# Optimization experiments

Hardware: AMD Instinct MI355X
Metric: run time of the kernel (lower is better)

## Reference

```python
import jax, jax.numpy as jnp
import numpy as np

IN_C = 256
OUT_C = 256
K_NUM = 6
EDGE_TYPE = 3


def setup_inputs() -> dict:
    key = jax.random.key(0)
    k1, k2, k3, k4, k5 = jax.random.split(key, 5)
    N, T, V = 32, 64, 25
    x = jax.random.normal(k1, (N, IN_C, T, V), dtype=jnp.float32)
    A = jax.random.uniform(k2, (K_NUM - EDGE_TYPE, V, V), dtype=jnp.float32)
    B = jax.random.uniform(k3, (N, EDGE_TYPE, V, V), dtype=jnp.float32)
    lamda_act = jnp.float32(0.5)
    # ConvTranspose2d with kernel (1,1), stride 1, no padding == pointwise matmul.
    # torch weight shape (in, out, 1, 1) -> store squeezed (in, out).
    W = jax.random.normal(k4, (IN_C, OUT_C * K_NUM), dtype=jnp.float32) * (1.0 / np.sqrt(IN_C))
    b = jax.random.normal(k5, (OUT_C * K_NUM,), dtype=jnp.float32) * 0.01
    return {"x": x, "A": A, "B": B, "lamda_act": lamda_act, "W": W, "b": b}


def reference(x, A, B, lamda_act, W, b):
    # pointwise transposed conv (1x1 kernel) -> channel matmul
    y = jnp.einsum('nctv,co->notv', x, W) + b[None, :, None, None]  # [N, K*C_out, T, V]
    n, kc, t, v = y.shape
    y = y.reshape(n, K_NUM, kc // K_NUM, t, v)
    x1 = jnp.einsum('nkctv,kvw->nctw', y[:, :K_NUM - EDGE_TYPE], A)
    x2 = jnp.einsum('nkctv,nkvw->nctw', y[:, K_NUM - EDGE_TYPE:], B)
    x_sum = x1 + x2 * lamda_act
    return (x_sum, A)
```

## Files before the change

### kernel.cpp

```cpp
#include <hip/hip_runtime.h>
#include <hip/hip_bf16.h>
#include <stdint.h>

typedef __bf16 bf16_t;
typedef bf16_t bf16x8 __attribute__((ext_vector_type(8)));
typedef float f32x4 __attribute__((ext_vector_type(4)));

#define DEVI static __device__ __forceinline__

constexpr int NB = 32, CIN = 256, COUT = 256, KNUM = 6, ET = 3, TDIM = 64, VV = 25;
constexpr int KD   = KNUM * CIN;
constexpr long OUT0 = (long)NB * COUT * TDIM * VV;
constexpr int ACNT = ET * VV * VV;

constexpr int NSTEP = 24;
constexpr int WP3_CHUNKS = NSTEP * 2048;
constexpr size_t WP3_BYTES  = (size_t)WP3_CHUNKS * 16;
constexpr size_t BIAS_OFF   = WP3_BYTES;
constexpr size_t BIAS_BYTES = (size_t)NB * VV * COUT * 4;
constexpr size_t WS_NEED    = BIAS_OFF + BIAS_BYTES;

DEVI unsigned packbf(float lo, float hi) {
  unsigned short a = __builtin_bit_cast(unsigned short, (bf16_t)lo);
  unsigned short b = __builtin_bit_cast(unsigned short, (bf16_t)hi);
  return ((unsigned)b << 16) | (unsigned)a;
}

__global__ __launch_bounds__(256) void prep_kernel(
    const float* __restrict__ A, const float* __restrict__ Bm,
    const float* __restrict__ lam_p, const float* __restrict__ W,
    const float* __restrict__ bvec, bf16_t* __restrict__ wp3,
    float* __restrict__ biasmat, float* __restrict__ outA)
{
  int idx = blockIdx.x * 256 + threadIdx.x;
  constexpr int S1 = WP3_CHUNKS;
  constexpr int S2 = S1 + NB * VV * COUT;
  constexpr int S3 = S2 + ACNT;
  if (idx < S1) {
    int s  = idx >> 11;
    int r  = idx & 2047;
    int mi = r >> 7;
    int kk = (r >> 6) & 1;
    int ln = r & 63;
    int lg = ln >> 4, lw = ln & 15;
    int cb = s / 6, k = s - cb * 6;
    int cibase = cb * 64 + (lg + 4 * kk) * 8;
    int col = (k << 8) + mi * 16 + lw;
    bf16_t* dst = wp3 + ((long)idx << 3);
    #pragma unroll
    for (int e = 0; e < 8; ++e)
      dst[e] = (bf16_t)W[(cibase + e) * KD + col];
  } else if (idx < S2) {
    int j = idx - S1;
    int c = j & 255;
    int nw = j >> 8;
    int w = nw % VV;
    int n = nw / VV;
    float lam = lam_p[0];
    float s = 0.f;
    for (int k = 0; k < KNUM; ++k) {
      float sk = 0.f;
      if (k < ET) {
        for (int v = 0; v < VV; ++v) sk += A[(k * VV + v) * VV + w];
      } else {
        for (int v = 0; v < VV; ++v) sk += Bm[(((n * ET) + (k - ET)) * VV + v) * VV + w];
        sk *= lam;
      }
      s += bvec[(k << 8) + c] * sk;
    }
    biasmat[j] = s;
  } else if (idx < S3) {
    int j = idx - S2;
    outA[j] = A[j];
  }
}

__global__ __launch_bounds__(512, 2) void fused_kernel(
    const float* __restrict__ x, const float* __restrict__ A,
    const float* __restrict__ Bm, const float* __restrict__ lam_p,
    const bf16_t* __restrict__ wp3, const float* __restrict__ biasmat,
    float* __restrict__ out)
{
  __shared__ bf16_t Bs[2 * 128 * 64];
  __shared__ bf16_t Xs[256 * 32];
  __shared__ bf16_t Ms[KNUM * 32 * 32];

  const int b = blockIdx.x;
  const int n = b >> 4;
  const int t0 = (b & 15) << 2;
  const int tid = threadIdx.x;
  const int wv = tid >> 6, ln = tid & 63;
  const int lw = ln & 15, lg = ln >> 4;
  const float lam = lam_p[0];

  for (int i = tid; i < KNUM * 32 * 32; i += 512) {
    int R = i >> 5, v = i & 31;
    int k = i >> 10, w = (i >> 5) & 31;
    float val = 0.f;
    if (w < VV && v < VV)
      val = (k < ET) ? A[(k * VV + v) * VV + w]
                     : lam * Bm[(((n * ET) + (k - ET)) * VV + v) * VV + w];
    int sw2 = (w & 3) ^ ((w >> 2) & 3);
    int byteoff = R * 64 + ((((v >> 3) ^ sw2) & 3) << 4) + ((v & 7) << 1);
    *(bf16_t*)((char*)Ms + byteoff) = (bf16_t)val;
  }

  f32x4 acc[4][4] = {};
  const int m_base = (wv >> 1) * 64;
  const int mb4 = (wv >> 1) * 4;
  const int n_base = (wv & 1) * 64;
  const f32x4 z4 = {0.f, 0.f, 0.f, 0.f};
  const int msw2 = (lw & 3) ^ ((lw >> 2) & 3);

  for (int cb = 0; cb < 4; ++cb) {
    if (tid < 256) {
      int ci = tid >> 2, dt = tid & 3;
      const float* xp = x + ((long)(n * CIN + cb * 64 + ci) * TDIM + t0 + dt) * VV;
      float xv[25];
      #pragma unroll
      for (int v = 0; v < VV; ++v) xv[v] = xp[v];
      int row = dt * 64 + ci;
      int sw = (row & 3) ^ ((row >> 2) & 3);
      #pragma unroll
      for (int g = 0; g < 4; ++g) {
        char* base = (char*)Xs + row * 64 + ((g ^ sw) & 3) * 16;
        #pragma unroll
        for (int p = 0; p < 4; ++p) {
          int v0 = g * 8 + p * 2;
          float lo = (v0     < VV) ? xv[v0 < VV ? v0 : 0]     : 0.f;
          float hi = (v0 + 1 < VV) ? xv[v0 + 1 < VV ? v0 + 1 : 0] : 0.f;
          *(unsigned*)(base + p * 4) = packbf(lo, hi);
        }
      }
    }
    __syncthreads();

    for (int k = 0; k < KNUM; ++k) {
      const int s = cb * 6 + k;
      const int buf = (s & 1) * (128 * 64);
      bf16x8 af2[2][4];
      const bf16_t* wpS = wp3 + (((long)s * 2048 + (long)mb4 * 128 + ln) << 3);
      #pragma unroll
      for (int kk = 0; kk < 2; ++kk)
        #pragma unroll
        for (int i = 0; i < 4; ++i)
          af2[kk][i] = *(const bf16x8*)(wpS + ((i * 128 + kk * 64) << 3));

      bf16x8 mb0 = *(const bf16x8*)((const char*)Ms + (k * 32 + lw) * 64 + (((lg ^ msw2) & 3) << 4));
      bf16x8 mb1 = *(const bf16x8*)((const char*)Ms + (k * 32 + 16 + lw) * 64 + (((lg ^ msw2) & 3) << 4));
      #pragma unroll
      for (int rt = 0; rt < 2; ++rt) {
        int arow = wv * 32 + rt * 16 + lw;
        int sw = (arow & 3) ^ ((arow >> 2) & 3);
        bf16x8 af = *(const bf16x8*)((const char*)Xs + arow * 64 + ((lg ^ sw) & 3) * 16);
        f32x4 d0 = __builtin_amdgcn_mfma_f32_16x16x32_bf16(af, mb0, z4, 0, 0, 0);
        f32x4 d1 = __builtin_amdgcn_mfma_f32_16x16x32_bf16(af, mb1, z4, 0, 0, 0);
        int rbase = wv * 32 + rt * 16 + (lg << 2);
        int dt = rbase >> 6, ci0 = rbase & 63;
        int r0 = dt * 32 + lw;
        int g0 = ((ci0 >> 3) ^ (r0 & 7)) & 7;
        char* c0 = (char*)(Bs + buf) + r0 * 128 + (g0 << 4) + ((ci0 << 1) & 15);
        *(unsigned*)(c0)     = packbf(d0[0], d0[1]);
        *(unsigned*)(c0 + 4) = packbf(d0[2], d0[3]);
        int r1 = r0 + 16;
        char* c1 = (char*)(Bs + buf) + r1 * 128 + (g0 << 4) + ((ci0 << 1) & 15);
        *(unsigned*)(c1)     = packbf(d1[0], d1[1]);
        *(unsigned*)(c1 + 4) = packbf(d1[2], d1[3]);
      }
      __syncthreads();

      __builtin_amdgcn_s_setprio(1);
      #pragma unroll
      for (int kk = 0; kk < 2; ++kk) {
        bf16x8 bf2[4];
        #pragma unroll
        for (int j = 0; j < 4; ++j) {
          int rr = n_base + j * 16 + lw;
          int gg = ((kk * 4 + lg) ^ (rr & 7)) & 7;
          bf2[j] = *(const bf16x8*)((const char*)(Bs + buf) + rr * 128 + (gg << 4));
        }
        #pragma unroll
        for (int i = 0; i < 4; ++i)
          #pragma unroll
          for (int j = 0; j < 4; ++j)
            acc[i][j] = __builtin_amdgcn_mfma_f32_16x16x32_bf16(af2[kk][i], bf2[j], acc[i][j], 0, 0, 0);
      }
      __builtin_amdgcn_s_setprio(0);
    }
  }

  #pragma unroll
  for (int j = 0; j < 4; ++j) {
    int colb = n_base + j * 16 + lw;
    int dt = colb >> 5, w = colb & 31;
    if (w < VV) {
      float* ob = out + (long)n * 409600 + (t0 + dt) * 25 + w;
      const float* brow = biasmat + (n * 25 + w) * 256;
      #pragma unroll
      for (int i = 0; i < 4; ++i) {
        int mb = m_base + i * 16 + (lg << 2);
        #pragma unroll
        for (int r = 0; r < 4; ++r) {
          int m = mb + r;
          ob[(long)m * 1600] = acc[i][j][r] + brow[m];
        }
      }
    }
  }
}

__global__ __launch_bounds__(256) void fallback_kernel(
    const float* __restrict__ x, const float* __restrict__ A,
    const float* __restrict__ Bm, const float* __restrict__ lam_p,
    const float* __restrict__ W, const float* __restrict__ bvec,
    float* __restrict__ out)
{
  __shared__ __align__(16) float xs[CIN][28];
  __shared__ __align__(16) float Ms[KNUM][VV][28];
  const int nt = blockIdx.x;
  const int n = nt >> 6, t = nt & 63;
  const int tid = threadIdx.x;
  const float lam = lam_p[0];

  const float* xp = x + (((long)(n * CIN + tid) * TDIM + t) * VV);
  #pragma unroll
  for (int v = 0; v < VV; ++v) xs[tid][v] = xp[v];
  xs[tid][25] = xs[tid][26] = xs[tid][27] = 0.f;
  for (int i = tid; i < KNUM * VV * VV; i += 256) {
    int k = i / (VV * VV);
    int r = i - k * VV * VV;
    int v = r / VV;
    int w = r - v * VV;
    Ms[k][v][w] = (k < ET) ? A[(k * VV + v) * VV + w]
                           : lam * Bm[(((n * ET) + (k - ET)) * VV + v) * VV + w];
    if (w == 24) { Ms[k][v][25] = Ms[k][v][26] = Ms[k][v][27] = 0.f; }
  }
  __syncthreads();

  float oacc[28] = {};
  for (int k = 0; k < KNUM; ++k) {
    float yv[28];
    float bv = bvec[(k << 8) + tid];
    #pragma unroll
    for (int v = 0; v < 28; ++v) yv[v] = 0.f;
    for (int ci = 0; ci < CIN; ++ci) {
      float wl = W[ci * KD + (k << 8) + tid];
      const f32x4* x4 = (const f32x4*)&xs[ci][0];
      #pragma unroll
      for (int q = 0; q < 7; ++q) {
        f32x4 xv = x4[q];
        yv[q*4+0] += wl*xv[0]; yv[q*4+1] += wl*xv[1];
        yv[q*4+2] += wl*xv[2]; yv[q*4+3] += wl*xv[3];
      }
    }
    #pragma unroll
    for (int v = 0; v < VV; ++v) {
      float yvv = yv[v] + bv;
      const f32x4* m4 = (const f32x4*)&Ms[k][v][0];
      #pragma unroll
      for (int q = 0; q < 7; ++q) {
        f32x4 mv = m4[q];
        oacc[q*4+0] += yvv*mv[0]; oacc[q*4+1] += yvv*mv[1];
        oacc[q*4+2] += yvv*mv[2]; oacc[q*4+3] += yvv*mv[3];
      }
    }
  }
  float* op = out + (((long)(n * COUT + tid) * TDIM + t) * VV);
  #pragma unroll
  for (int w = 0; w < VV; ++w) op[w] = oacc[w];
}

__global__ void copyA_kernel(const float* __restrict__ A, float* __restrict__ outA) {
  int i = blockIdx.x * 256 + threadIdx.x;
  if (i < ACNT) outA[i] = A[i];
}

extern "C" void kernel_launch(void* const* d_in, const int* in_sizes, int n_in,
                              void* d_out, int out_size, void* d_ws, size_t ws_size,
                              hipStream_t stream) {
  const float* x   = (const float*)d_in[0];
  const float* A   = (const float*)d_in[1];
  const float* Bm  = (const float*)d_in[2];
  const float* lam = (const float*)d_in[3];
  const float* W   = (const float*)d_in[4];
  const float* bv  = (const float*)d_in[5];
  float* out = (float*)d_out;

  if (d_ws != nullptr && ws_size >= WS_NEED) {
    bf16_t* wp3     = (bf16_t*)d_ws;
    float*  biasmat = (float*)((char*)d_ws + BIAS_OFF);
    constexpr int PREP_ITEMS = WP3_CHUNKS + NB * VV * COUT + ACNT;
    prep_kernel<<<(PREP_ITEMS + 255) / 256, 256, 0, stream>>>(A, Bm, lam, W, bv, wp3, biasmat, out + OUT0);
    fused_kernel<<<NB * 16, 512, 0, stream>>>(x, A, Bm, lam, wp3, biasmat, out);
  } else {
    fallback_kernel<<<NB * TDIM, 256, 0, stream>>>(x, A, Bm, lam, W, bv, out);
    copyA_kernel<<<(ACNT + 255) / 256, 256, 0, stream>>>(A, out + OUT0);
  }
}
```

Measured before the change: 84.55 us.

## Feed first-stage MFMA outputs directly as B-fragments, removing Bs LDS round trip

Each wave now recomputes the graph-mixing MFMA (X times adjacency) for exactly the columns it needs and repacks the fp32 results into bf16 B-operand fragments in registers. This drops the Bs shared-memory staging buffer and the per-step __syncthreads, and Xs rows are permuted so the accumulator layout lines up with the operand layout. The cost is redundant first-stage MFMAs: both waves sharing an n-range recompute the same tile, roughly doubling that small stage. Weight fragments are now loaded per kk, and the k loop is kept rolled.

```diff
diff --git a/kernel.cpp b/kernel.cpp
--- a/kernel.cpp
+++ b/kernel.cpp
@@ -24,6 +24,13 @@
   unsigned short a = __builtin_bit_cast(unsigned short, (bf16_t)lo);
   unsigned short b = __builtin_bit_cast(unsigned short, (bf16_t)hi);
   return ((unsigned)b << 16) | (unsigned)a;
+}
+
+DEVI bf16x8 pack8(f32x4 a, f32x4 b) {
+  union { unsigned u[4]; bf16x8 v; } u;
+  u.u[0] = packbf(a[0], a[1]); u.u[1] = packbf(a[2], a[3]);
+  u.u[2] = packbf(b[0], b[1]); u.u[3] = packbf(b[2], b[3]);
+  return u.v;
 }
 
 __global__ __launch_bounds__(256) void prep_kernel(
@@ -81,7 +88,6 @@
     const bf16_t* __restrict__ wp3, const float* __restrict__ biasmat,
     float* __restrict__ out)
 {
-  __shared__ bf16_t Bs[2 * 128 * 64];
   __shared__ bf16_t Xs[256 * 32];
   __shared__ bf16_t Ms[KNUM * 32 * 32];
 
@@ -109,17 +115,20 @@
   const int m_base = (wv >> 1) * 64;
   const int mb4 = (wv >> 1) * 4;
   const int n_base = (wv & 1) * 64;
+  const int dtb = (wv & 1) * 2;
   const f32x4 z4 = {0.f, 0.f, 0.f, 0.f};
   const int msw2 = (lw & 3) ^ ((lw >> 2) & 3);
 
   for (int cb = 0; cb < 4; ++cb) {
+    __syncthreads();
     if (tid < 256) {
       int ci = tid >> 2, dt = tid & 3;
       const float* xp = x + ((long)(n * CIN + cb * 64 + ci) * TDIM + t0 + dt) * VV;
       float xv[25];
       #pragma unroll
       for (int v = 0; v < VV; ++v) xv[v] = xp[v];
-      int row = dt * 64 + ci;
+      int kk = ci >> 5, rem = ci & 31, q = rem >> 3, r = rem & 7;
+      int row = dt * 64 + kk * 32 + (r >> 2) * 16 + q * 4 + (r & 3);
       int sw = (row & 3) ^ ((row >> 2) & 3);
       #pragma unroll
       for (int g = 0; g < 4; ++g) {
@@ -135,57 +144,44 @@
     }
     __syncthreads();
 
+    #pragma unroll 1
     for (int k = 0; k < KNUM; ++k) {
       const int s = cb * 6 + k;
-      const int buf = (s & 1) * (128 * 64);
-      bf16x8 af2[2][4];
-      const bf16_t* wpS = wp3 + (((long)s * 2048 + (long)mb4 * 128 + ln) << 3);
-      #pragma unroll
-      for (int kk = 0; kk < 2; ++kk)
-        #pragma unroll
-        for (int i = 0; i < 4; ++i)
-          af2[kk][i] = *(const bf16x8*)(wpS + ((i * 128 + kk * 64) << 3));
-
       bf16x8 mb0 = *(const bf16x8*)((const char*)Ms + (k * 32 + lw) * 64 + (((lg ^ msw2) & 3) << 4));
       bf16x8 mb1 = *(const bf16x8*)((const char*)Ms + (k * 32 + 16 + lw) * 64 + (((lg ^ msw2) & 3) << 4));
-      #pragma unroll
-      for (int rt = 0; rt < 2; ++rt) {
-        int arow = wv * 32 + rt * 16 + lw;
-        int sw = (arow & 3) ^ ((arow >> 2) & 3);
-        bf16x8 af = *(const bf16x8*)((const char*)Xs + arow * 64 + ((lg ^ sw) & 3) * 16);
-        f32x4 d0 = __builtin_amdgcn_mfma_f32_16x16x32_bf16(af, mb0, z4, 0, 0, 0);
-        f32x4 d1 = __builtin_amdgcn_mfma_f32_16x16x32_bf16(af, mb1, z4, 0, 0, 0);
-        int rbase = wv * 32 + rt * 16 + (lg << 2);
-        int dt = rbase >> 6, ci0 = rbase & 63;
-        int r0 = dt * 32 + lw;
-        int g0 = ((ci0 >> 3) ^ (r0 & 7)) & 7;
-        char* c0 = (char*)(Bs + buf) + r0 * 128 + (g0 << 4) + ((ci0 << 1) & 15);
-        *(unsigned*)(c0)     = packbf(d0[0], d0[1]);
-        *(unsigned*)(c0 + 4) = packbf(d0[2], d0[3]);
-        int r1 = r0 + 16;
-        char* c1 = (char*)(Bs + buf) + r1 * 128 + (g0 << 4) + ((ci0 << 1) & 15);
-        *(unsigned*)(c1)     = packbf(d1[0], d1[1]);
-        *(unsigned*)(c1 + 4) = packbf(d1[2], d1[3]);
-      }
-      __syncthreads();
-
-      __builtin_amdgcn_s_setprio(1);
+      const bf16_t* wpS = wp3 + (((long)s * 2048 + (long)mb4 * 128 + ln) << 3);
+
       #pragma unroll
       for (int kk = 0; kk < 2; ++kk) {
-        bf16x8 bf2[4];
-        #pragma unroll
-        for (int j = 0; j < 4; ++j) {
-          int rr = n_base + j * 16 + lw;
-          int gg = ((kk * 4 + lg) ^ (rr & 7)) & 7;
-          bf2[j] = *(const bf16x8*)((const char*)(Bs + buf) + rr * 128 + (gg << 4));
+        bf16x8 af2[4];
+        #pragma unroll
+        for (int i = 0; i < 4; ++i)
+          af2[i] = *(const bf16x8*)(wpS + ((i * 128 + kk * 64) << 3));
+
+        bf16x8 bfrag[4];
+        #pragma unroll
+        for (int dtl = 0; dtl < 2; ++dtl) {
+          int ra = (dtb + dtl) * 64 + kk * 32 + lw;
+          int swa = (ra & 3) ^ ((ra >> 2) & 3);
+          int off = ((lg ^ swa) & 3) << 4;
+          bf16x8 afa = *(const bf16x8*)((const char*)Xs + ra * 64 + off);
+          bf16x8 afb = *(const bf16x8*)((const char*)Xs + (ra + 16) * 64 + off);
+          f32x4 da0 = __builtin_amdgcn_mfma_f32_16x16x32_bf16(afa, mb0, z4, 0, 0, 0);
+          f32x4 db0 = __builtin_amdgcn_mfma_f32_16x16x32_bf16(afb, mb0, z4, 0, 0, 0);
+          f32x4 da1 = __builtin_amdgcn_mfma_f32_16x16x32_bf16(afa, mb1, z4, 0, 0, 0);
+          f32x4 db1 = __builtin_amdgcn_mfma_f32_16x16x32_bf16(afb, mb1, z4, 0, 0, 0);
+          bfrag[dtl * 2 + 0] = pack8(da0, db0);
+          bfrag[dtl * 2 + 1] = pack8(da1, db1);
         }
+
+        __builtin_amdgcn_s_setprio(1);
         #pragma unroll
         for (int i = 0; i < 4; ++i)
           #pragma unroll
           for (int j = 0; j < 4; ++j)
-            acc[i][j] = __builtin_amdgcn_mfma_f32_16x16x32_bf16(af2[kk][i], bf2[j], acc[i][j], 0, 0, 0);
-      }
-      __builtin_amdgcn_s_setprio(0);
+            acc[i][j] = __builtin_amdgcn_mfma_f32_16x16x32_bf16(af2[i], bfrag[j], acc[i][j], 0, 0, 0);
+        __builtin_amdgcn_s_setprio(0);
+      }
     }
   }
 
```

New measurement: 94.75 us. 1.12x slower.

## Split output channels across two blocks and stage epilogue through LDS for coalesced stores

Applied to the files above, without the earlier changes.

Doubles the grid so each block computes half of the 256 output channels, halving accumulator registers and raising launch bounds to 4 waves-per-SIMD occupancy. The x tile load is spread across all 512 threads instead of 256. The epilogue now stages accumulators through shared memory and writes contiguous runs of the output, replacing strided per-element stores. In exchange, the first-stage x·M product and the x load are recomputed by both halves, so that work is duplicated.

```diff
diff --git a/kernel.cpp b/kernel.cpp
--- a/kernel.cpp
+++ b/kernel.cpp
@@ -75,19 +75,21 @@
   }
 }
 
-__global__ __launch_bounds__(512, 2) void fused_kernel(
+__global__ __launch_bounds__(512, 4) void fused_kernel(
     const float* __restrict__ x, const float* __restrict__ A,
     const float* __restrict__ Bm, const float* __restrict__ lam_p,
     const bf16_t* __restrict__ wp3, const float* __restrict__ biasmat,
     float* __restrict__ out)
 {
-  __shared__ bf16_t Bs[2 * 128 * 64];
-  __shared__ bf16_t Xs[256 * 32];
-  __shared__ bf16_t Ms[KNUM * 32 * 32];
+  __shared__ __align__(16) bf16_t Bs[2 * 128 * 64];
+  __shared__ __align__(16) bf16_t Xs[256 * 32];
+  __shared__ __align__(16) bf16_t Ms[KNUM * 32 * 32];
 
   const int b = blockIdx.x;
-  const int n = b >> 4;
-  const int t0 = (b & 15) << 2;
+  const int half = b >> 9;
+  const int rest = b & 511;
+  const int n = rest >> 4;
+  const int t0 = (rest & 15) << 2;
   const int tid = threadIdx.x;
   const int wv = tid >> 6, ln = tid & 63;
   const int lw = ln & 15, lg = ln >> 4;
@@ -105,45 +107,53 @@
     *(bf16_t*)((char*)Ms + byteoff) = (bf16_t)val;
   }
 
-  f32x4 acc[4][4] = {};
-  const int m_base = (wv >> 1) * 64;
-  const int mb4 = (wv >> 1) * 4;
+  f32x4 acc[2][4] = {};
+  const int miB = half * 8 + (wv >> 1) * 2;
   const int n_base = (wv & 1) * 64;
   const f32x4 z4 = {0.f, 0.f, 0.f, 0.f};
   const int msw2 = (lw & 3) ^ ((lw >> 2) & 3);
 
   for (int cb = 0; cb < 4; ++cb) {
-    if (tid < 256) {
-      int ci = tid >> 2, dt = tid & 3;
-      const float* xp = x + ((long)(n * CIN + cb * 64 + ci) * TDIM + t0 + dt) * VV;
-      float xv[25];
-      #pragma unroll
-      for (int v = 0; v < VV; ++v) xv[v] = xp[v];
+    __syncthreads();
+    {
+      int jj = tid & 255, gh = tid >> 8;
+      int ci = jj >> 2, dt = jj & 3;
+      const float* xp = x + ((long)(n * CIN + cb * 64 + ci) * TDIM + t0 + dt) * VV + gh * 16;
+      float xv[16];
+      #pragma unroll
+      for (int v = 0; v < 16; ++v) xv[v] = 0.f;
+      if (gh == 0) {
+        #pragma unroll
+        for (int v = 0; v < 16; ++v) xv[v] = xp[v];
+      } else {
+        #pragma unroll
+        for (int v = 0; v < 9; ++v) xv[v] = xp[v];
+      }
       int row = dt * 64 + ci;
       int sw = (row & 3) ^ ((row >> 2) & 3);
       #pragma unroll
-      for (int g = 0; g < 4; ++g) {
+      for (int g2 = 0; g2 < 2; ++g2) {
+        int g = gh * 2 + g2;
         char* base = (char*)Xs + row * 64 + ((g ^ sw) & 3) * 16;
         #pragma unroll
         for (int p = 0; p < 4; ++p) {
-          int v0 = g * 8 + p * 2;
-          float lo = (v0     < VV) ? xv[v0 < VV ? v0 : 0]     : 0.f;
-          float hi = (v0 + 1 < VV) ? xv[v0 + 1 < VV ? v0 + 1 : 0] : 0.f;
-          *(unsigned*)(base + p * 4) = packbf(lo, hi);
+          int vl = g2 * 8 + p * 2;
+          *(unsigned*)(base + p * 4) = packbf(xv[vl], xv[vl + 1]);
         }
       }
     }
     __syncthreads();
 
+    #pragma unroll 1
     for (int k = 0; k < KNUM; ++k) {
       const int s = cb * 6 + k;
       const int buf = (s & 1) * (128 * 64);
-      bf16x8 af2[2][4];
-      const bf16_t* wpS = wp3 + (((long)s * 2048 + (long)mb4 * 128 + ln) << 3);
+      bf16x8 af2[2][2];
+      const bf16_t* wpS = wp3 + (((long)s * 2048 + (long)miB * 128 + ln) << 3);
       #pragma unroll
       for (int kk = 0; kk < 2; ++kk)
         #pragma unroll
-        for (int i = 0; i < 4; ++i)
+        for (int i = 0; i < 2; ++i)
           af2[kk][i] = *(const bf16x8*)(wpS + ((i * 128 + kk * 64) << 3));
 
       bf16x8 mb0 = *(const bf16x8*)((const char*)Ms + (k * 32 + lw) * 64 + (((lg ^ msw2) & 3) << 4));
@@ -152,20 +162,18 @@
       for (int rt = 0; rt < 2; ++rt) {
         int arow = wv * 32 + rt * 16 + lw;
         int sw = (arow & 3) ^ ((arow >> 2) & 3);
-        bf16x8 af = *(const bf16x8*)((const char*)Xs + arow * 64 + ((lg ^ sw) & 3) * 16);
+        int off = ((lg ^ sw) & 3) << 4;
+        bf16x8 af = *(const bf16x8*)((const char*)Xs + arow * 64 + off);
         f32x4 d0 = __builtin_amdgcn_mfma_f32_16x16x32_bf16(af, mb0, z4, 0, 0, 0);
         f32x4 d1 = __builtin_amdgcn_mfma_f32_16x16x32_bf16(af, mb1, z4, 0, 0, 0);
         int rbase = wv * 32 + rt * 16 + (lg << 2);
         int dt = rbase >> 6, ci0 = rbase & 63;
         int r0 = dt * 32 + lw;
         int g0 = ((ci0 >> 3) ^ (r0 & 7)) & 7;
-        char* c0 = (char*)(Bs + buf) + r0 * 128 + (g0 << 4) + ((ci0 << 1) & 15);
-        *(unsigned*)(c0)     = packbf(d0[0], d0[1]);
-        *(unsigned*)(c0 + 4) = packbf(d0[2], d0[3]);
-        int r1 = r0 + 16;
-        char* c1 = (char*)(Bs + buf) + r1 * 128 + (g0 << 4) + ((ci0 << 1) & 15);
-        *(unsigned*)(c1)     = packbf(d1[0], d1[1]);
-        *(unsigned*)(c1 + 4) = packbf(d1[2], d1[3]);
+        uint2 p0; p0.x = packbf(d0[0], d0[1]); p0.y = packbf(d0[2], d0[3]);
+        *(uint2*)((char*)(Bs + buf) + r0 * 128 + (g0 << 4) + ((ci0 << 1) & 15)) = p0;
+        uint2 p1; p1.x = packbf(d1[0], d1[1]); p1.y = packbf(d1[2], d1[3]);
+        *(uint2*)((char*)(Bs + buf) + (r0 + 16) * 128 + (g0 << 4) + ((ci0 << 1) & 15)) = p1;
       }
       __syncthreads();
 
@@ -180,7 +188,7 @@
           bf2[j] = *(const bf16x8*)((const char*)(Bs + buf) + rr * 128 + (gg << 4));
         }
         #pragma unroll
-        for (int i = 0; i < 4; ++i)
+        for (int i = 0; i < 2; ++i)
           #pragma unroll
           for (int j = 0; j < 4; ++j)
             acc[i][j] = __builtin_amdgcn_mfma_f32_16x16x32_bf16(af2[kk][i], bf2[j], acc[i][j], 0, 0, 0);
@@ -189,23 +197,41 @@
     }
   }
 
-  #pragma unroll
-  for (int j = 0; j < 4; ++j) {
-    int colb = n_base + j * 16 + lw;
-    int dt = colb >> 5, w = colb & 31;
-    if (w < VV) {
-      float* ob = out + (long)n * 409600 + (t0 + dt) * 25 + w;
-      const float* brow = biasmat + (n * 25 + w) * 256;
-      #pragma unroll
-      for (int i = 0; i < 4; ++i) {
-        int mb = m_base + i * 16 + (lg << 2);
-        #pragma unroll
-        for (int r = 0; r < 4; ++r) {
-          int m = mb + r;
-          ob[(long)m * 1600] = acc[i][j][r] + brow[m];
+  __syncthreads();
+  float* eb = (float*)Bs;
+  const int q = wv >> 1;
+  const int slot = q & 1;
+  #pragma unroll 1
+  for (int rnd = 0; rnd < 2; ++rnd) {
+    if ((q >> 1) == rnd) {
+      #pragma unroll
+      for (int i = 0; i < 2; ++i)
+        #pragma unroll
+        for (int j = 0; j < 4; ++j) {
+          int col = n_base + j * 16 + lw;
+          int dt = col >> 5, w = col & 31;
+          if (w < VV) {
+            #pragma unroll
+            for (int r = 0; r < 4; ++r) {
+              int cl = i * 16 + (lg << 2) + r;
+              eb[(slot * 32 + cl) * 124 + dt * 31 + w] = acc[i][j][r];
+            }
+          }
         }
-      }
-    }
+    }
+    __syncthreads();
+    {
+      int ch = tid >> 8, c = (tid >> 3) & 31, dt = (tid >> 1) & 3, wh = tid & 1;
+      int qq = rnd * 2 + ch;
+      int cg = half * 128 + qq * 32 + c;
+      const float* src = eb + (ch * 32 + c) * 124 + dt * 31 + wh * 13;
+      float* dst = out + (long)n * 409600 + (long)cg * 1600 + (t0 + dt) * 25 + wh * 13;
+      const float* bb = biasmat + n * 25 * 256 + cg;
+      int cnt = wh ? 12 : 13;
+      for (int it = 0; it < cnt; ++it)
+        dst[it] = src[it] + bb[(wh * 13 + it) * 256];
+    }
+    __syncthreads();
   }
 }
 
@@ -291,7 +317,7 @@
     float*  biasmat = (float*)((char*)d_ws + BIAS_OFF);
     constexpr int PREP_ITEMS = WP3_CHUNKS + NB * VV * COUT + ACNT;
     prep_kernel<<<(PREP_ITEMS + 255) / 256, 256, 0, stream>>>(A, Bm, lam, W, bv, wp3, biasmat, out + OUT0);
-    fused_kernel<<<NB * 16, 512, 0, stream>>>(x, A, Bm, lam, wp3, biasmat, out);
+    fused_kernel<<<2 * NB * 16, 512, 0, stream>>>(x, A, Bm, lam, wp3, biasmat, out);
   } else {
     fallback_kernel<<<NB * TDIM, 256, 0, stream>>>(x, A, Bm, lam, W, bv, out);
     copyA_kernel<<<(ACNT + 255) / 256, 256, 0, stream>>>(A, out + OUT0);
```

Result: slower. 122.8 us (+45.2%).

## Halve per-block time tile to double grid size and raise occupancy

Applied to the files above, without the earlier changes.

Each block now covers 2 time steps instead of 4, so the grid doubles to NB*32 blocks and shared buffers and accumulators shrink by half. Launch bounds move to 4 blocks per CU, the x-load is split across two threads per row, and the k loop is kept rolled. This aims to fill the CUs better and hide latency. The cost is that the W fragments are reloaded from global memory twice as often, the per-step barriers are amortised over less MMA work, and the tighter register budget may cause spills.

```diff
diff --git a/kernel.cpp b/kernel.cpp
--- a/kernel.cpp
+++ b/kernel.cpp
@@ -75,19 +75,19 @@
   }
 }
 
-__global__ __launch_bounds__(512, 2) void fused_kernel(
+__global__ __launch_bounds__(512, 4) void fused_kernel(
     const float* __restrict__ x, const float* __restrict__ A,
     const float* __restrict__ Bm, const float* __restrict__ lam_p,
     const bf16_t* __restrict__ wp3, const float* __restrict__ biasmat,
     float* __restrict__ out)
 {
-  __shared__ bf16_t Bs[2 * 128 * 64];
-  __shared__ bf16_t Xs[256 * 32];
-  __shared__ bf16_t Ms[KNUM * 32 * 32];
+  __shared__ __align__(16) bf16_t Bs[2 * 64 * 64];
+  __shared__ __align__(16) bf16_t Xs[128 * 32];
+  __shared__ __align__(16) bf16_t Ms[KNUM * 32 * 32];
 
   const int b = blockIdx.x;
-  const int n = b >> 4;
-  const int t0 = (b & 15) << 2;
+  const int n = b >> 5;
+  const int t0 = (b & 31) << 1;
   const int tid = threadIdx.x;
   const int wv = tid >> 6, ln = tid & 63;
   const int lw = ln & 15, lg = ln >> 4;
@@ -105,39 +105,47 @@
     *(bf16_t*)((char*)Ms + byteoff) = (bf16_t)val;
   }
 
-  f32x4 acc[4][4] = {};
+  f32x4 acc[4][2] = {};
   const int m_base = (wv >> 1) * 64;
   const int mb4 = (wv >> 1) * 4;
-  const int n_base = (wv & 1) * 64;
+  const int n_base = (wv & 1) * 32;
   const f32x4 z4 = {0.f, 0.f, 0.f, 0.f};
   const int msw2 = (lw & 3) ^ ((lw >> 2) & 3);
 
   for (int cb = 0; cb < 4; ++cb) {
+    __syncthreads();
     if (tid < 256) {
-      int ci = tid >> 2, dt = tid & 3;
-      const float* xp = x + ((long)(n * CIN + cb * 64 + ci) * TDIM + t0 + dt) * VV;
-      float xv[25];
-      #pragma unroll
-      for (int v = 0; v < VV; ++v) xv[v] = xp[v];
-      int row = dt * 64 + ci;
+      int row = tid >> 1, gh = tid & 1;
+      int dt = row >> 6, ci = row & 63;
+      const float* xp = x + ((long)(n * CIN + cb * 64 + ci) * TDIM + t0 + dt) * VV + gh * 16;
+      float xv[16];
+      #pragma unroll
+      for (int v = 0; v < 16; ++v) xv[v] = 0.f;
+      if (gh == 0) {
+        #pragma unroll
+        for (int v = 0; v < 16; ++v) xv[v] = xp[v];
+      } else {
+        #pragma unroll
+        for (int v = 0; v < 9; ++v) xv[v] = xp[v];
+      }
       int sw = (row & 3) ^ ((row >> 2) & 3);
       #pragma unroll
-      for (int g = 0; g < 4; ++g) {
+      for (int g2 = 0; g2 < 2; ++g2) {
+        int g = gh * 2 + g2;
         char* base = (char*)Xs + row * 64 + ((g ^ sw) & 3) * 16;
         #pragma unroll
         for (int p = 0; p < 4; ++p) {
-          int v0 = g * 8 + p * 2;
-          float lo = (v0     < VV) ? xv[v0 < VV ? v0 : 0]     : 0.f;
-          float hi = (v0 + 1 < VV) ? xv[v0 + 1 < VV ? v0 + 1 : 0] : 0.f;
-          *(unsigned*)(base + p * 4) = packbf(lo, hi);
+          int vl = g2 * 8 + p * 2;
+          *(unsigned*)(base + p * 4) = packbf(xv[vl], xv[vl + 1]);
         }
       }
     }
     __syncthreads();
 
+    #pragma unroll 1
     for (int k = 0; k < KNUM; ++k) {
       const int s = cb * 6 + k;
-      const int buf = (s & 1) * (128 * 64);
+      const int buf = (s & 1) * (64 * 64);
       bf16x8 af2[2][4];
       const bf16_t* wpS = wp3 + (((long)s * 2048 + (long)mb4 * 128 + ln) << 3);
       #pragma unroll
@@ -148,22 +156,21 @@
 
       bf16x8 mb0 = *(const bf16x8*)((const char*)Ms + (k * 32 + lw) * 64 + (((lg ^ msw2) & 3) << 4));
       bf16x8 mb1 = *(const bf16x8*)((const char*)Ms + (k * 32 + 16 + lw) * 64 + (((lg ^ msw2) & 3) << 4));
-      #pragma unroll
-      for (int rt = 0; rt < 2; ++rt) {
-        int arow = wv * 32 + rt * 16 + lw;
+      {
+        int arow = wv * 16 + lw;
         int sw = (arow & 3) ^ ((arow >> 2) & 3);
-        bf16x8 af = *(const bf16x8*)((const char*)Xs + arow * 64 + ((lg ^ sw) & 3) * 16);
+        int off = ((lg ^ sw) & 3) << 4;
+        bf16x8 af = *(const bf16x8*)((const char*)Xs + arow * 64 + off);
         f32x4 d0 = __builtin_amdgcn_mfma_f32_16x16x32_bf16(af, mb0, z4, 0, 0, 0);
         f32x4 d1 = __builtin_amdgcn_mfma_f32_16x16x32_bf16(af, mb1, z4, 0, 0, 0);
-        int rbase = wv * 32 + rt * 16 + (lg << 2);
+        int rbase = wv * 16 + (lg << 2);
         int dt = rbase >> 6, ci0 = rbase & 63;
         int r0 = dt * 32 + lw;
         int g0 = ((ci0 >> 3) ^ (r0 & 7)) & 7;
         char* c0 = (char*)(Bs + buf) + r0 * 128 + (g0 << 4) + ((ci0 << 1) & 15);
         *(unsigned*)(c0)     = packbf(d0[0], d0[1]);
         *(unsigned*)(c0 + 4) = packbf(d0[2], d0[3]);
-        int r1 = r0 + 16;
-        char* c1 = (char*)(Bs + buf) + r1 * 128 + (g0 << 4) + ((ci0 << 1) & 15);
+        char* c1 = (char*)(Bs + buf) + (r0 + 16) * 128 + (g0 << 4) + ((ci0 << 1) & 15);
         *(unsigned*)(c1)     = packbf(d1[0], d1[1]);
         *(unsigned*)(c1 + 4) = packbf(d1[2], d1[3]);
       }
@@ -172,9 +179,9 @@
       __builtin_amdgcn_s_setprio(1);
       #pragma unroll
       for (int kk = 0; kk < 2; ++kk) {
-        bf16x8 bf2[4];
-        #pragma unroll
-        for (int j = 0; j < 4; ++j) {
+        bf16x8 bf2[2];
+        #pragma unroll
+        for (int j = 0; j < 2; ++j) {
           int rr = n_base + j * 16 + lw;
           int gg = ((kk * 4 + lg) ^ (rr & 7)) & 7;
           bf2[j] = *(const bf16x8*)((const char*)(Bs + buf) + rr * 128 + (gg << 4));
@@ -182,7 +189,7 @@
         #pragma unroll
         for (int i = 0; i < 4; ++i)
           #pragma unroll
-          for (int j = 0; j < 4; ++j)
+          for (int j = 0; j < 2; ++j)
             acc[i][j] = __builtin_amdgcn_mfma_f32_16x16x32_bf16(af2[kk][i], bf2[j], acc[i][j], 0, 0, 0);
       }
       __builtin_amdgcn_s_setprio(0);
@@ -190,7 +197,7 @@
   }
 
   #pragma unroll
-  for (int j = 0; j < 4; ++j) {
+  for (int j = 0; j < 2; ++j) {
     int colb = n_base + j * 16 + lw;
     int dt = colb >> 5, w = colb & 31;
     if (w < VV) {
@@ -291,7 +298,7 @@
     float*  biasmat = (float*)((char*)d_ws + BIAS_OFF);
     constexpr int PREP_ITEMS = WP3_CHUNKS + NB * VV * COUT + ACNT;
     prep_kernel<<<(PREP_ITEMS + 255) / 256, 256, 0, stream>>>(A, Bm, lam, W, bv, wp3, biasmat, out + OUT0);
-    fused_kernel<<<NB * 16, 512, 0, stream>>>(x, A, Bm, lam, wp3, biasmat, out);
+    fused_kernel<<<NB * 32, 512, 0, stream>>>(x, A, Bm, lam, wp3, biasmat, out);
   } else {
     fallback_kernel<<<NB * TDIM, 256, 0, stream>>>(x, A, Bm, lam, W, bv, out);
     copyA_kernel<<<(ACNT + 255) / 256, 256, 0, stream>>>(A, out + OUT0);
```

New measurement: 92.35 us. 9.2% more time.
